# Performance work log

Measured on AMD Instinct MI355X. Metric: run time of the kernel, lower is better.

## Reference

```python
import jax, jax.numpy as jnp
import numpy as np

DIM = 1024
HEADS = 16
HEAD_DIM = DIM // HEADS
DFF = 4 * DIM
BASE_THETA, K_DOP, K_NOR, K_SERO = 0.5, 0.2, 0.15, 0.1
EPS = 1e-5


def _layernorm(x, g, b):
    mu = jnp.mean(x, axis=-1, keepdims=True)
    var = jnp.var(x, axis=-1, keepdims=True)
    return (x - mu) * jax.lax.rsqrt(var + EPS) * g + b


def setup_inputs() -> dict:
    key = jax.random.key(0)
    ks = jax.random.split(key, 16)
    s = 0.02
    d = {
        'x': jax.random.normal(ks[0], (2, 2048, DIM), dtype=jnp.float32),
        'ln1_g': jnp.ones((DIM,), jnp.float32),
        'ln1_b': jnp.zeros((DIM,), jnp.float32),
        'qkv_w': jax.random.normal(ks[1], (DIM, 3 * DIM), jnp.float32) * s,
        'qkv_b': jnp.zeros((3 * DIM,), jnp.float32),
        'proj_w': jax.random.normal(ks[2], (DIM, DIM), jnp.float32) * s,
        'proj_b': jnp.zeros((DIM,), jnp.float32),
        'kq_w': jax.random.normal(ks[3], (DIM, DIM), jnp.float32) * s,
        'kq_b': jnp.zeros((DIM,), jnp.float32),
        'kk_w': jax.random.normal(ks[4], (DIM, DIM), jnp.float32) * s,
        'kk_b': jnp.zeros((DIM,), jnp.float32),
        'kv_w': jax.random.normal(ks[5], (DIM, DIM), jnp.float32) * s,
        'kv_b': jnp.zeros((DIM,), jnp.float32),
        'ko_w': jax.random.normal(ks[6], (DIM, DIM), jnp.float32) * s,
        'ko_b': jnp.zeros((DIM,), jnp.float32),
        'ln2_g': jnp.ones((DIM,), jnp.float32),
        'ln2_b': jnp.zeros((DIM,), jnp.float32),
        'fc1_w': jax.random.normal(ks[7], (DIM, DFF), jnp.float32) * s,
        'fc1_b': jnp.zeros((DFF,), jnp.float32),
        'fc2_w': jax.random.normal(ks[8], (DFF, DIM), jnp.float32) * s,
        'fc2_b': jnp.zeros((DIM,), jnp.float32),
    }
    return d


def _mha(x, qkv_w, qkv_b, proj_w, proj_b):
    B, N, C = x.shape
    qkv = (x @ qkv_w + qkv_b).reshape(B, N, 3, HEADS, HEAD_DIM)
    q, k, v = qkv[:, :, 0], qkv[:, :, 1], qkv[:, :, 2]  # [B,N,H,Hd]
    scale = HEAD_DIM ** -0.5
    attn = jnp.einsum('bnhd,bmhd->bhnm', q, k) * scale
    attn = jax.nn.softmax(attn, axis=-1)
    out = jnp.einsum('bhnm,bmhd->bnhd', attn, v).reshape(B, N, C)
    return out @ proj_w + proj_b


def _kernel_attn(x, kq_w, kq_b, kk_w, kk_b, kv_w, kv_b, ko_w, ko_b):
    q = x @ kq_w + kq_b
    k = x @ kk_w + kk_b
    v = x @ kv_w + kv_b
    qk = jnp.einsum('bnc,bmc->bnm', q, k)
    theta = (BASE_THETA + K_DOP * jax.nn.sigmoid(qk)
             + K_NOR * jnp.tanh(qk) + K_SERO * jax.nn.relu(qk))
    attn = jax.nn.softmax(theta, axis=-1)
    out = jnp.einsum('bnm,bmc->bnc', attn, v)
    return out @ ko_w + ko_b


def reference(x, ln1_g, ln1_b, qkv_w, qkv_b, proj_w, proj_b,
              kq_w, kq_b, kk_w, kk_b, kv_w, kv_b, ko_w, ko_b,
              ln2_g, ln2_b, fc1_w, fc1_b, fc2_w, fc2_b):
    x = x + _mha(_layernorm(x, ln1_g, ln1_b), qkv_w, qkv_b, proj_w, proj_b)
    x = x + _kernel_attn(x, kq_w, kq_b, kk_w, kk_b, kv_w, kv_b, ko_w, ko_b)
    h = _layernorm(x, ln2_g, ln2_b)
    h = jax.nn.gelu(h @ fc1_w + fc1_b, approximate=False) @ fc2_w + fc2_b
    return x + h
```

## Files before the change

### kernel.cpp

```cpp
#include <hip/hip_runtime.h>
#include <math.h>


#define DIMC   1024
#define NTOK   4096
#define SEQ    2048
#define NHEADS 16
#define DFFC   4096
#define QSCALE 0.125f

typedef unsigned short u16;
typedef __attribute__((ext_vector_type(8))) short s16x8;
typedef __attribute__((ext_vector_type(4))) float f32x4;
#define MFMA16(a,b,c) __builtin_amdgcn_mfma_f32_16x16x32_bf16(a,b,c,0,0,0)

__device__ __forceinline__ float b2f(u16 u){ return __uint_as_float(((unsigned int)u)<<16); }
__device__ __forceinline__ u16 f2b(float f){
  unsigned int u = __float_as_uint(f);
  u += 0x7fffu + ((u>>16)&1u);
  return (u16)(u>>16);
}
__device__ __forceinline__ unsigned int pkbf(float a, float b){
  unsigned int r;
  asm("v_cvt_pk_bf16_f32 %0, %1, %2" : "=v"(r) : "v"(a), "v"(b));
  return r;
}
__device__ __forceinline__ float frcp(float x){
  float r;
  asm("v_rcp_f32 %0, %1" : "=v"(r) : "v"(x));
  return r;
}

__device__ __forceinline__ float ldIn(const void* base, long idx, int f32){
  return f32 ? ((const float*)base)[idx] : b2f(((const u16*)base)[idx]);
}
__device__ __forceinline__ float4 ldIn4(const void* base, long idx, int f32){
  if (f32) return *(const float4*)((const float*)base + idx);
  ushort4 u = *(const ushort4*)((const u16*)base + idx);
  return make_float4(b2f(u.x), b2f(u.y), b2f(u.z), b2f(u.w));
}
__device__ __forceinline__ void ld8(const void* base, long idx, int f32, float* v){
  if (f32){
    float4 a = *(const float4*)((const float*)base + idx);
    float4 b = *(const float4*)((const float*)base + idx + 4);
    v[0]=a.x; v[1]=a.y; v[2]=a.z; v[3]=a.w;
    v[4]=b.x; v[5]=b.y; v[6]=b.z; v[7]=b.w;
  } else {
    ushort4 a = *(const ushort4*)((const u16*)base + idx);
    ushort4 b = *(const ushort4*)((const u16*)base + idx + 4);
    v[0]=b2f(a.x); v[1]=b2f(a.y); v[2]=b2f(a.z); v[3]=b2f(a.w);
    v[4]=b2f(b.x); v[5]=b2f(b.y); v[6]=b2f(b.z); v[7]=b2f(b.w);
  }
}
__device__ __forceinline__ void st8(void* base, long idx, int f32, const float* v){
  if (f32){
    *(float4*)((float*)base + idx)     = make_float4(v[0],v[1],v[2],v[3]);
    *(float4*)((float*)base + idx + 4) = make_float4(v[4],v[5],v[6],v[7]);
  } else {
    unsigned int q0 = (unsigned int)f2b(v[0]) | ((unsigned int)f2b(v[1])<<16);
    unsigned int q1 = (unsigned int)f2b(v[2]) | ((unsigned int)f2b(v[3])<<16);
    unsigned int q2 = (unsigned int)f2b(v[4]) | ((unsigned int)f2b(v[5])<<16);
    unsigned int q3 = (unsigned int)f2b(v[6]) | ((unsigned int)f2b(v[7])<<16);
    *(uint4*)((u16*)base + idx) = make_uint4(q0,q1,q2,q3);
  }
}

__device__ __forceinline__ float waveSum(float v){
  #pragma unroll
  for (int off=32; off>0; off>>=1) v += __shfl_xor(v, off, 64);
  return v;
}

__device__ __forceinline__ void async16(const u16* g, u16* l){
  __builtin_amdgcn_global_load_lds(
      (const __attribute__((address_space(1))) unsigned int*)g,
      (__attribute__((address_space(3))) unsigned int*)l, 16, 0, 0);
}

__global__ void detect_kernel(const void* ones, int* flag){
  if (threadIdx.x == 0 && blockIdx.x == 0){
    unsigned int w = *(const unsigned int*)ones;
    *flag = (w == 0x3F803F80u) ? 0 : 1;
  }
}

__global__ __launch_bounds__(256)
void transpose_w(const void* __restrict__ in, u16* __restrict__ out,
                 const int* __restrict__ flagp, int K, int N)
{
  __shared__ u16 t[32][36];
  const int fl = *flagp;
  const int n0 = blockIdx.x*32, k0 = blockIdx.y*32;
  const int tx = threadIdx.x & 31, ty = threadIdx.x >> 5;
  #pragma unroll
  for (int r = ty; r < 32; r += 8)
    t[r][tx] = f2b(ldIn(in, (long)(k0+r)*N + n0 + tx, fl));
  __syncthreads();
  #pragma unroll
  for (int r = ty; r < 32; r += 8)
    out[(long)(n0+r)*K + k0 + tx] = t[tx][r];
}

__global__ __launch_bounds__(256)
void transpose_w3(const void* in0, const void* in1, const void* in2,
                  u16* __restrict__ out, const int* __restrict__ flagp)
{
  __shared__ u16 t[32][36];
  const int fl = *flagp;
  const void* in = (blockIdx.z==0) ? in0 : ((blockIdx.z==1) ? in1 : in2);
  u16* o = out + (long)blockIdx.z*1048576L;
  const int n0 = blockIdx.x*32, k0 = blockIdx.y*32;
  const int tx = threadIdx.x & 31, ty = threadIdx.x >> 5;
  #pragma unroll
  for (int r = ty; r < 32; r += 8)
    t[r][tx] = f2b(ldIn(in, (long)(k0+r)*1024 + n0 + tx, fl));
  __syncthreads();
  #pragma unroll
  for (int r = ty; r < 32; r += 8)
    o[(long)(n0+r)*1024 + k0 + tx] = t[tx][r];
}

template<int BM, int MODE, int ACT, int NW>
__global__ __launch_bounds__(NW*64)
void gemm_mfma(const u16* __restrict__ A, const u16* __restrict__ BT,
               const void* __restrict__ bias, const void* __restrict__ bias2,
               const void* __restrict__ bias3, const void* res,
               void* C, u16* Cv, const int* __restrict__ flagp, int cExt,
               int M, int N, int K, int lda, int ldb, int ldc,
               long sA, long sB, long sC)
{
  constexpr int DEPTH = (BM==128) ? 1 : 3;
  constexpr int BUFS = (BM+128)*64;
  constexpr int ST   = BM*132;
  constexpr int LSZ  = (DEPTH*BUFS > ST) ? DEPTH*BUFS : ST;
  __shared__ u16 lds[LSZ];

  const int fl = *flagp;
  const int fC = cExt ? fl : 0;
  const int z = blockIdx.z;
  A += (long)z*sA; BT += (long)z*sB;
  const long coff = (long)z*sC;
  const int m0 = blockIdx.x*BM, n0 = blockIdx.y*128;
  const int tid = threadIdx.x, w = tid>>6, l = tid&63;
  const int lr = l&15, lq = l>>4;
  constexpr int MW  = (NW==8) ? 4 : 2;
  constexpr int FM  = BM/MW/16;
  constexpr int ANI = BM/8/NW;
  constexpr int BNI = 16/NW;
  constexpr int LCNT= ANI+BNI;
  const int wm = (w&(MW-1))*(BM/MW), wn = (w/MW)*64;

  const int rq = l>>3;
  const int cperm = (l&7) ^ rq;
  const u16* pa = A  + (long)(m0 + rq)*lda + cperm*8;
  const u16* pb = BT + (long)(n0 + rq)*ldb + cperm*8;

  f32x4 acc[FM][4];
  f32x4 osum[FM];
  #pragma unroll
  for (int i=0;i<FM;i++){
    osum[i] = (f32x4){0.f,0.f,0.f,0.f};
    #pragma unroll
    for (int j=0;j<4;j++) acc[i][j] = (f32x4){0.f,0.f,0.f,0.f};
  }

  auto stage = [&](u16* buf){
    u16* As = buf;
    u16* Bs = buf + BM*64;
    #pragma unroll
    for (int p=0;p<ANI;p++){
      const int ia = p*NW + w;
      async16(pa + (long)ia*8*lda, &As[ia*512]);
    }
    #pragma unroll
    for (int p=0;p<BNI;p++){
      const int ib = p*NW + w;
      async16(pb + (long)ib*8*ldb, &Bs[ib*512]);
    }
    pa += 64; pb += 64;
  };

  auto compute = [&](const u16* As){
    const u16* Bs = As + BM*64;
    const int swz = lr & 7;
    #pragma unroll
    for (int h=0; h<2; h++){
      s16x8 af[FM], bf[4];
      const int slot = ((h*4 + lq) ^ swz) << 3;
      #pragma unroll
      for (int i=0;i<FM;i++)
        af[i] = *(const s16x8*)&As[(wm + i*16 + lr)*64 + slot];
      #pragma unroll
      for (int j=0;j<4;j++)
        bf[j] = *(const s16x8*)&Bs[(wn + j*16 + lr)*64 + slot];
      __builtin_amdgcn_s_setprio(1);
      #pragma unroll
      for (int i=0;i<FM;i++)
        #pragma unroll
        for (int j=0;j<4;j++) acc[i][j] = MFMA16(af[i], bf[j], acc[i][j]);
      if constexpr (MODE==5){
        const s16x8 onesv = (s16x8){0x3F80,0x3F80,0x3F80,0x3F80,
                                    0x3F80,0x3F80,0x3F80,0x3F80};
        #pragma unroll
        for (int i=0;i<FM;i++) osum[i] = MFMA16(af[i], onesv, osum[i]);
      }
      __builtin_amdgcn_s_setprio(0);
    }
  };

  const int nk = K >> 6;

  if constexpr (DEPTH == 3){
    auto waitL = [&](){
      if constexpr (LCNT==3)      asm volatile("s_waitcnt vmcnt(3)" ::: "memory");
      else if constexpr (LCNT==6) asm volatile("s_waitcnt vmcnt(6)" ::: "memory");
      else                        asm volatile("s_waitcnt vmcnt(8)" ::: "memory");
      __builtin_amdgcn_s_barrier();
    };
    stage(lds);
    stage(lds + BUFS);
    int cur = 0;
    for (int t = 0; t < nk-2; ++t){
      waitL();
      int nxt = cur+2; if (nxt >= 3) nxt -= 3;
      stage(lds + nxt*BUFS);
      compute(lds + cur*BUFS);
      cur = (cur==2) ? 0 : cur+1;
    }
    waitL();
    compute(lds + cur*BUFS);
    cur = (cur==2) ? 0 : cur+1;
    asm volatile("s_waitcnt vmcnt(0)" ::: "memory");
    __builtin_amdgcn_s_barrier();
    compute(lds + cur*BUFS);
    __syncthreads();
  } else {
    for (int t = 0; t < nk; ++t){
      stage(lds);
      asm volatile("s_waitcnt vmcnt(0)" ::: "memory");
      __builtin_amdgcn_s_barrier();
      compute(lds);
      __syncthreads();
    }
  }

  if constexpr (MODE==5){
    #pragma unroll
    for (int i=0;i<FM;i++)
      #pragma unroll
      for (int r=0;r<4;r++){
        float inv = 1.f / osum[i][r];
        #pragma unroll
        for (int j=0;j<4;j++) acc[i][j][r] *= inv;
      }
  }

  const bool vtr = (MODE==1) && (n0 >= 2048);
  #pragma unroll
  for (int i=0;i<FM;i++)
    #pragma unroll
    for (int j=0;j<4;j++)
      #pragma unroll
      for (int r=0;r<4;r++){
        const u16 bv16 = f2b(acc[i][j][r]);
        if (vtr)
          lds[(wn + j*16 + lr)*132 + wm + i*16 + lq*4 + r] = bv16;
        else
          lds[(wm + i*16 + lq*4 + r)*132 + wn + j*16 + lr] = bv16;
      }
  __syncthreads();

  constexpr int RPP = NW*4;
  const int trow = tid >> 4, tcol = (tid & 15)*8;
  const int gcol = n0 + tcol;

  if (vtr){
    const int bidx = m0 >> 11;
    const int tb = (m0 & 2047) + tcol;
    #pragma unroll
    for (int p=0; p<BM/RPP; p++){
      const int ch = p*RPP + trow;
      float bv = ldIn(bias3, n0 - 2048 + ch, fl);
      float v[8];
      #pragma unroll
      for (int e=0;e<8;e++) v[e] = b2f(lds[ch*132 + tcol + e]) + bv;
      st8(Cv, (long)bidx*2097152L + (long)(n0 - 2048 + ch)*2048 + tb, 0, v);
    }
    return;
  }

  #pragma unroll
  for (int p=0; p<BM/RPP; p++){
    const int row = p*RPP + trow;
    const long grow = m0 + row;
    float v[8];
    #pragma unroll
    for (int e=0;e<8;e++) v[e] = b2f(lds[row*132 + tcol + e]);

    if (MODE == 2){
      #pragma unroll
      for (int e=0;e<8;e++){
        float q = v[e];
        float En = __expf(-q);
        float sig = frcp(1.f + En);
        float t2 = fminf(En*En, 3.0e38f);
        float th = (1.f - t2) * frcp(1.f + t2);
        v[e] = __expf(0.5f + 0.2f*sig + 0.15f*th + 0.1f*fmaxf(q,0.f));
      }
      st8(C, coff + grow*ldc + gcol, 0, v);
    } else if (MODE == 1){
      const void* bb = (n0 < 1024) ? bias : bias2;
      const int cofs = (n0 < 1024) ? 0 : 1024;
      float bv[8]; ld8(bb, gcol - cofs, fl, bv);
      #pragma unroll
      for (int e=0;e<8;e++) v[e] += bv[e];
      st8(C, grow*2048 + gcol, 0, v);
    } else {
      if (bias){
        float bv[8]; ld8(bias, gcol, fl, bv);
        #pragma unroll
        for (int e=0;e<8;e++) v[e] += bv[e];
      }
      if (MODE == 3 && gcol < 1024){
        #pragma unroll
        for (int e=0;e<8;e++) v[e] *= QSCALE;
      }
      if (ACT==1){
        #pragma unroll
        for (int e=0;e<8;e++){
          float u = v[e];
          float y = 1.5957691216f*u*(1.f + 0.044715f*u*u);
          v[e] = u / (1.f + __expf(-y));
        }
      }
      const long idx = coff + grow*ldc + gcol;
      if (res){
        float rv[8]; ld8(res, idx, fl, rv);
        #pragma unroll
        for (int e=0;e<8;e++) v[e] += rv[e];
      }
      st8(C, idx, fC, v);
      if (MODE == 4)
        st8(Cv, grow*1024 + gcol, 0, v);
    }
  }
}

__global__ __launch_bounds__(256)
void ln_kernel(const void* __restrict__ in, const void* __restrict__ g,
               const void* __restrict__ b, u16* __restrict__ outp,
               const int* __restrict__ flagp, int inFlagged)
{
  const int fl = *flagp;
  const int fin = inFlagged ? fl : 0;
  const int row = blockIdx.x;
  const int tid = threadIdx.x;
  float4 xv = ldIn4(in, (long)row*DIMC + tid*4, fin);
  float v0=xv.x, v1=xv.y, v2=xv.z, v3=xv.w;
  float s  = v0+v1+v2+v3;
  float s2 = v0*v0+v1*v1+v2*v2+v3*v3;
  s = waveSum(s); s2 = waveSum(s2);
  __shared__ float sh[8];
  int w = tid>>6, ln = tid&63;
  if (ln==0){ sh[w]=s; sh[4+w]=s2; }
  __syncthreads();
  float ts  = sh[0]+sh[1]+sh[2]+sh[3];
  float ts2 = sh[4]+sh[5]+sh[6]+sh[7];
  float mu  = ts * (1.f/1024.f);
  float var = ts2 * (1.f/1024.f) - mu*mu;
  float rs  = rsqrtf(var + 1e-5f);
  int c = tid*4;
  float4 gv = ldIn4(g, c, fl);
  float4 bv = ldIn4(b, c, fl);
  ushort4 o;
  o.x = f2b((v0-mu)*rs*gv.x + bv.x);
  o.y = f2b((v1-mu)*rs*gv.y + bv.y);
  o.z = f2b((v2-mu)*rs*gv.z + bv.z);
  o.w = f2b((v3-mu)*rs*gv.w + bv.w);
  *(ushort4*)(outp + (long)row*DIMC + c) = o;
}

__global__ __launch_bounds__(512)
void mha_flash(const u16* __restrict__ qkv, u16* __restrict__ outp)
{
  __shared__ u16 Kl[2][64][72];
  __shared__ u16 Vt[2][64][72];
  __shared__ u16 Pl[8][16][72];
  const int h  = blockIdx.y;
  const int bb = blockIdx.z;
  const int q0 = blockIdx.x * 128;
  const int tid = threadIdx.x, lane = tid & 63, w = tid >> 6;
  const int lr = lane & 15, lq = lane >> 4;
  const long tokBase = (long)bb * SEQ;

  s16x8 qf0, qf1;
  {
    const u16* qp = qkv + (tokBase + q0 + w*16 + lr)*3072 + h*64 + lq*8;
    qf0 = *(const s16x8*)qp;
    qf1 = *(const s16x8*)(qp + 32);
  }
  f32x4 o[4];
  #pragma unroll
  for (int d=0;d<4;d++) o[d] = (f32x4){0.f,0.f,0.f,0.f};
  f32x4 osum = (f32x4){0.f,0.f,0.f,0.f};
  const s16x8 onesv = (s16x8){0x3F80,0x3F80,0x3F80,0x3F80,0x3F80,0x3F80,0x3F80,0x3F80};

  const int kk = tid >> 3, kd = (tid & 7) * 8;
  const bool doV = (tid < 256);
  const int p2 = tid & 31, dg = (tid >> 5) & 7;

  uint4 kr, vA, vB;
  const u16* kbase = qkv + (tokBase + kk)*3072 + 1024 + h*64 + kd;
  const u16* vbase = qkv + (tokBase + 2*p2)*3072 + 2048 + h*64 + dg*8;

  auto ldKV = [&](int k0){
    kr = *(const uint4*)(kbase + (long)k0*3072);
    if (doV){
      const u16* vp = vbase + (long)k0*3072;
      vA = *(const uint4*)vp;
      vB = *(const uint4*)(vp + 3072);
    }
  };
  auto wrKV = [&](int bi){
    *(uint4*)&Kl[bi][kk][kd] = kr;
    if (doV){
      unsigned int pk;
      #pragma unroll
      for (int jj=0;jj<4;jj++){
        pk = ((const u16*)&vA)[jj] | ((unsigned int)((const u16*)&vB)[jj] << 16);
        *(unsigned int*)&Vt[bi][dg*8+jj][2*p2] = pk;
        pk = ((const u16*)&vA)[4+jj] | ((unsigned int)((const u16*)&vB)[4+jj] << 16);
        *(unsigned int*)&Vt[bi][dg*8+4+jj][2*p2] = pk;
      }
    }
  };

  ldKV(0);
  int bi = 0;
  for (int k0 = 0; k0 < SEQ; k0 += 64){
    wrKV(bi);
    if (k0 + 64 < SEQ) ldKV(k0 + 64);
    __syncthreads();

    f32x4 s[4];
    #pragma unroll
    for (int c=0;c<4;c++){
      s[c] = (f32x4){0.f,0.f,0.f,0.f};
      s16x8 kf0 = *(const s16x8*)&Kl[bi][c*16+lr][lq*8];
      s16x8 kf1 = *(const s16x8*)&Kl[bi][c*16+lr][lq*8+32];
      __builtin_amdgcn_s_setprio(1);
      s[c] = MFMA16(qf0, kf0, s[c]);
      s[c] = MFMA16(qf1, kf1, s[c]);
      __builtin_amdgcn_s_setprio(0);
    }
    #pragma unroll
    for (int c=0;c<4;c++){
      float p0 = __expf(s[c][0]);
      float p1 = __expf(s[c][1]);
      float p2v = __expf(s[c][2]);
      float p3 = __expf(s[c][3]);
      unsigned int a01 = pkbf(p0, p1);
      unsigned int a23 = pkbf(p2v, p3);
      u16* pr = &Pl[w][lq*4][c*16+lr];
      pr[0]   = (u16)a01;
      pr[72]  = (u16)(a01>>16);
      pr[144] = (u16)a23;
      pr[216] = (u16)(a23>>16);
    }
    s16x8 pf0 = *(const s16x8*)&Pl[w][lr][lq*8];
    s16x8 pf1 = *(const s16x8*)&Pl[w][lr][32+lq*8];
    __builtin_amdgcn_s_setprio(1);
    osum = MFMA16(pf0, onesv, osum);
    osum = MFMA16(pf1, onesv, osum);
    __builtin_amdgcn_s_setprio(0);
    #pragma unroll
    for (int d=0;d<4;d++){
      s16x8 vf0 = *(const s16x8*)&Vt[bi][d*16+lr][lq*8];
      s16x8 vf1 = *(const s16x8*)&Vt[bi][d*16+lr][32+lq*8];
      __builtin_amdgcn_s_setprio(1);
      o[d] = MFMA16(pf0, vf0, o[d]);
      o[d] = MFMA16(pf1, vf1, o[d]);
      __builtin_amdgcn_s_setprio(0);
    }
    bi ^= 1;
  }

  #pragma unroll
  for (int r=0;r<4;r++){
    float inv = 1.f / osum[r];
    long row = (tokBase + q0 + w*16 + lq*4 + r) * (long)DIMC + h*64;
    unsigned int pk01 = pkbf(o[0][r]*inv, o[1][r]*inv);
    unsigned int pk23 = pkbf(o[2][r]*inv, o[3][r]*inv);
    outp[row + lr     ] = (u16)pk01;
    outp[row + lr + 16] = (u16)(pk01>>16);
    outp[row + lr + 32] = (u16)pk23;
    outp[row + lr + 48] = (u16)(pk23>>16);
  }
}

extern "C" void kernel_launch(void* const* d_in, const int* in_sizes, int n_in,
                              void* d_out, int out_size, void* d_ws, size_t ws_size,
                              hipStream_t stream)
{
  const void* x      = d_in[0];
  const void* ln1_g  = d_in[1];
  const void* ln1_b  = d_in[2];
  const void* qkv_w  = d_in[3];
  const void* qkv_b  = d_in[4];
  const void* proj_w = d_in[5];
  const void* proj_b = d_in[6];
  const void* kq_w   = d_in[7];
  const void* kq_b   = d_in[8];
  const void* kk_w   = d_in[9];
  const void* kk_b   = d_in[10];
  const void* kv_w   = d_in[11];
  const void* kv_b   = d_in[12];
  const void* ko_w   = d_in[13];
  const void* ko_b   = d_in[14];
  const void* ln2_g  = d_in[15];
  const void* ln2_b  = d_in[16];
  const void* fc1_w  = d_in[17];
  const void* fc1_b  = d_in[18];
  const void* fc2_w  = d_in[19];
  const void* fc2_b  = d_in[20];

  int* flag = (int*)d_ws;
  u16* Ar   = (u16*)((char*)d_ws + 64);
  u16* B0   = Ar + 4194304L;
  u16* QK   = B0;
  u16* Vt   = B0 + 8388608L;
  u16* C0   = B0 + 12582912L;
  u16* Sb   = C0;
  u16* WT   = C0;
  u16* WT2  = C0 + 4194304L;
  u16* AT   = C0 + 4194304L;
  u16* FC1  = B0;
  u16* Qr   = B0;

  dim3 blk(256);
  const void* np = nullptr;

  detect_kernel<<<1, 64, 0, stream>>>(ln1_g, flag);
  transpose_w<<<dim3(96,32), blk, 0, stream>>>(qkv_w, WT, flag, DIMC, 3*DIMC);
  ln_kernel<<<NTOK, blk, 0, stream>>>(x, ln1_g, ln1_b, Ar, flag, 1);
  gemm_mfma<128,3,0,4><<<dim3(32,24,1), blk, 0, stream>>>(
      Ar, WT, qkv_b, np, np, np, Qr, nullptr, flag, 0,
      NTOK, 3*DIMC, DIMC, DIMC, DIMC, 3*DIMC, 0,0,0);
  mha_flash<<<dim3(SEQ/128, NHEADS, 2), dim3(512), 0, stream>>>(Qr, AT);
  transpose_w<<<dim3(32,32), blk, 0, stream>>>(proj_w, WT, flag, DIMC, DIMC);
  gemm_mfma<64,4,0,8><<<dim3(64,8,1), dim3(512), 0, stream>>>(
      AT, WT, proj_b, np, np, x, d_out, Ar, flag, 1,
      NTOK, DIMC, DIMC, DIMC, DIMC, DIMC, 0,0,0);
  transpose_w3<<<dim3(32,32,3), blk, 0, stream>>>(kq_w, kk_w, kv_w, WT, flag);
  gemm_mfma<128,1,0,4><<<dim3(32,24,1), blk, 0, stream>>>(
      Ar, WT, kq_b, kk_b, kv_b, np, QK, Vt, flag, 0,
      NTOK, 3*DIMC, DIMC, DIMC, DIMC, 2048, 0,0,0);
  gemm_mfma<128,2,0,4><<<dim3(16,16,2), blk, 0, stream>>>(
      QK, QK + 1024, np, np, np, np, Sb, nullptr, flag, 0,
      SEQ, SEQ, DIMC, 2048, 2048, SEQ, 4194304L, 4194304L, 4194304L);
  gemm_mfma<64,5,0,8><<<dim3(32,8,2), dim3(512), 0, stream>>>(
      Sb, Vt, np, np, np, np, Ar, nullptr, flag, 0,
      SEQ, DIMC, SEQ, SEQ, SEQ, DIMC, 4194304L, 2097152L, 2097152L);
  transpose_w<<<dim3(32,32), blk, 0, stream>>>(ko_w, WT, flag, DIMC, DIMC);
  gemm_mfma<64,0,0,8><<<dim3(64,8,1), dim3(512), 0, stream>>>(
      Ar, WT, ko_b, np, np, d_out, d_out, nullptr, flag, 1,
      NTOK, DIMC, DIMC, DIMC, DIMC, DIMC, 0,0,0);
  ln_kernel<<<NTOK, blk, 0, stream>>>(d_out, ln2_g, ln2_b, Ar, flag, 1);
  transpose_w<<<dim3(128,32), blk, 0, stream>>>(fc1_w, WT2, flag, DIMC, DFFC);
  gemm_mfma<128,0,1,4><<<dim3(32,32,1), blk, 0, stream>>>(
      Ar, WT2, fc1_b, np, np, np, FC1, nullptr, flag, 0,
      NTOK, DFFC, DIMC, DIMC, DIMC, DFFC, 0,0,0);
  transpose_w<<<dim3(32,128), blk, 0, stream>>>(fc2_w, WT2, flag, DFFC, DIMC);
  gemm_mfma<64,0,0,8><<<dim3(64,8,1), dim3(512), 0, stream>>>(
      FC1, WT2, fc2_b, np, np, d_out, d_out, nullptr, flag, 1,
      NTOK, DIMC, DFFC, DFFC, DFFC, DIMC, 0,0,0);
}
```

Baseline: 571.6 us.

## Split MHA flash attention over key halves with a separate combine kernel

Splits the attention key range into two halves so the grid doubles from 512 to 1024 blocks. Each half writes unnormalized bf16 partial outputs and row sums to scratch buffers (d_out and Ar are reused), and a new combine kernel adds the halves and normalizes. The goal is better CU occupancy on a grid that was small relative to the GPU. In exchange it adds an extra kernel launch, extra global traffic and bf16 rounding of the partials, and it drops LDS double buffering in favour of two syncs per iteration.

```diff
diff --git a/kernel.cpp b/kernel.cpp
--- a/kernel.cpp
+++ b/kernel.cpp
@@ -381,17 +381,20 @@
 }
 
 __global__ __launch_bounds__(512)
-void mha_flash(const u16* __restrict__ qkv, u16* __restrict__ outp)
+void mha_split(const u16* __restrict__ qkv, u16* __restrict__ p0,
+               u16* __restrict__ p1, float* __restrict__ osums)
 {
-  __shared__ u16 Kl[2][64][72];
-  __shared__ u16 Vt[2][64][72];
+  __shared__ u16 Kl[64][72];
+  __shared__ u16 Vt[64][72];
   __shared__ u16 Pl[8][16][72];
   const int h  = blockIdx.y;
-  const int bb = blockIdx.z;
+  const int bb = blockIdx.z >> 1;
+  const int ks = blockIdx.z & 1;
   const int q0 = blockIdx.x * 128;
   const int tid = threadIdx.x, lane = tid & 63, w = tid >> 6;
   const int lr = lane & 15, lq = lane >> 4;
   const long tokBase = (long)bb * SEQ;
+  const long kBase   = tokBase + ks*1024;
 
   s16x8 qf0, qf1;
   {
@@ -410,8 +413,8 @@
   const int p2 = tid & 31, dg = (tid >> 5) & 7;
 
   uint4 kr, vA, vB;
-  const u16* kbase = qkv + (tokBase + kk)*3072 + 1024 + h*64 + kd;
-  const u16* vbase = qkv + (tokBase + 2*p2)*3072 + 2048 + h*64 + dg*8;
+  const u16* kbase = qkv + (kBase + kk)*3072 + 1024 + h*64 + kd;
+  const u16* vbase = qkv + (kBase + 2*p2)*3072 + 2048 + h*64 + dg*8;
 
   auto ldKV = [&](int k0){
     kr = *(const uint4*)(kbase + (long)k0*3072);
@@ -421,33 +424,33 @@
       vB = *(const uint4*)(vp + 3072);
     }
   };
-  auto wrKV = [&](int bi){
-    *(uint4*)&Kl[bi][kk][kd] = kr;
+  auto wrKV = [&](){
+    *(uint4*)&Kl[kk][kd] = kr;
     if (doV){
       unsigned int pk;
       #pragma unroll
       for (int jj=0;jj<4;jj++){
         pk = ((const u16*)&vA)[jj] | ((unsigned int)((const u16*)&vB)[jj] << 16);
-        *(unsigned int*)&Vt[bi][dg*8+jj][2*p2] = pk;
+        *(unsigned int*)&Vt[dg*8+jj][2*p2] = pk;
         pk = ((const u16*)&vA)[4+jj] | ((unsigned int)((const u16*)&vB)[4+jj] << 16);
-        *(unsigned int*)&Vt[bi][dg*8+4+jj][2*p2] = pk;
+        *(unsigned int*)&Vt[dg*8+4+jj][2*p2] = pk;
       }
     }
   };
 
   ldKV(0);
-  int bi = 0;
-  for (int k0 = 0; k0 < SEQ; k0 += 64){
-    wrKV(bi);
-    if (k0 + 64 < SEQ) ldKV(k0 + 64);
+  for (int k0 = 0; k0 < 1024; k0 += 64){
+    __syncthreads();
+    wrKV();
+    if (k0 + 64 < 1024) ldKV(k0 + 64);
     __syncthreads();
 
     f32x4 s[4];
     #pragma unroll
     for (int c=0;c<4;c++){
       s[c] = (f32x4){0.f,0.f,0.f,0.f};
-      s16x8 kf0 = *(const s16x8*)&Kl[bi][c*16+lr][lq*8];
-      s16x8 kf1 = *(const s16x8*)&Kl[bi][c*16+lr][lq*8+32];
+      s16x8 kf0 = *(const s16x8*)&Kl[c*16+lr][lq*8];
+      s16x8 kf1 = *(const s16x8*)&Kl[c*16+lr][lq*8+32];
       __builtin_amdgcn_s_setprio(1);
       s[c] = MFMA16(qf0, kf0, s[c]);
       s[c] = MFMA16(qf1, kf1, s[c]);
@@ -455,12 +458,12 @@
     }
     #pragma unroll
     for (int c=0;c<4;c++){
-      float p0 = __expf(s[c][0]);
-      float p1 = __expf(s[c][1]);
-      float p2v = __expf(s[c][2]);
-      float p3 = __expf(s[c][3]);
-      unsigned int a01 = pkbf(p0, p1);
-      unsigned int a23 = pkbf(p2v, p3);
+      float e0 = __expf(s[c][0]);
+      float e1 = __expf(s[c][1]);
+      float e2 = __expf(s[c][2]);
+      float e3 = __expf(s[c][3]);
+      unsigned int a01 = pkbf(e0, e1);
+      unsigned int a23 = pkbf(e2, e3);
       u16* pr = &Pl[w][lq*4][c*16+lr];
       pr[0]   = (u16)a01;
       pr[72]  = (u16)(a01>>16);
@@ -475,27 +478,48 @@
     __builtin_amdgcn_s_setprio(0);
     #pragma unroll
     for (int d=0;d<4;d++){
-      s16x8 vf0 = *(const s16x8*)&Vt[bi][d*16+lr][lq*8];
-      s16x8 vf1 = *(const s16x8*)&Vt[bi][d*16+lr][32+lq*8];
+      s16x8 vf0 = *(const s16x8*)&Vt[d*16+lr][lq*8];
+      s16x8 vf1 = *(const s16x8*)&Vt[d*16+lr][32+lq*8];
       __builtin_amdgcn_s_setprio(1);
       o[d] = MFMA16(pf0, vf0, o[d]);
       o[d] = MFMA16(pf1, vf1, o[d]);
       __builtin_amdgcn_s_setprio(0);
     }
-    bi ^= 1;
-  }
-
+  }
+
+  u16* pp = ks ? p1 : p0;
   #pragma unroll
   for (int r=0;r<4;r++){
-    float inv = 1.f / osum[r];
-    long row = (tokBase + q0 + w*16 + lq*4 + r) * (long)DIMC + h*64;
-    unsigned int pk01 = pkbf(o[0][r]*inv, o[1][r]*inv);
-    unsigned int pk23 = pkbf(o[2][r]*inv, o[3][r]*inv);
-    outp[row + lr     ] = (u16)pk01;
-    outp[row + lr + 16] = (u16)(pk01>>16);
-    outp[row + lr + 32] = (u16)pk23;
-    outp[row + lr + 48] = (u16)(pk23>>16);
-  }
+    long row = tokBase + q0 + w*16 + lq*4 + r;
+    long base = row * (long)DIMC + h*64;
+    unsigned int pk01 = pkbf(o[0][r], o[1][r]);
+    unsigned int pk23 = pkbf(o[2][r], o[3][r]);
+    pp[base + lr     ] = (u16)pk01;
+    pp[base + lr + 16] = (u16)(pk01>>16);
+    pp[base + lr + 32] = (u16)pk23;
+    pp[base + lr + 48] = (u16)(pk23>>16);
+    if (lr == 0)
+      osums[((long)ks*4096 + row)*16 + h] = osum[r];
+  }
+}
+
+__global__ __launch_bounds__(256)
+void mha_combine(const u16* __restrict__ p0, const u16* __restrict__ p1,
+                 const float* __restrict__ osums, u16* __restrict__ outp)
+{
+  const long row = blockIdx.x;
+  const int c = threadIdx.x * 4;
+  const int h = c >> 6;
+  float s = osums[row*16 + h] + osums[(4096 + row)*16 + h];
+  float inv = 1.f / s;
+  ushort4 a = *(const ushort4*)(p0 + row*DIMC + c);
+  ushort4 b = *(const ushort4*)(p1 + row*DIMC + c);
+  ushort4 o;
+  o.x = f2b((b2f(a.x)+b2f(b.x))*inv);
+  o.y = f2b((b2f(a.y)+b2f(b.y))*inv);
+  o.z = f2b((b2f(a.z)+b2f(b.z))*inv);
+  o.w = f2b((b2f(a.w)+b2f(b.w))*inv);
+  *(ushort4*)(outp + row*DIMC + c) = o;
 }
 
 extern "C" void kernel_launch(void* const* d_in, const int* in_sizes, int n_in,
@@ -536,6 +560,7 @@
   u16* AT   = C0 + 4194304L;
   u16* FC1  = B0;
   u16* Qr   = B0;
+  float* OS = (float*)C0;
 
   dim3 blk(256);
   const void* np = nullptr;
@@ -546,7 +571,9 @@
   gemm_mfma<128,3,0,4><<<dim3(32,24,1), blk, 0, stream>>>(
       Ar, WT, qkv_b, np, np, np, Qr, nullptr, flag, 0,
       NTOK, 3*DIMC, DIMC, DIMC, DIMC, 3*DIMC, 0,0,0);
-  mha_flash<<<dim3(SEQ/128, NHEADS, 2), dim3(512), 0, stream>>>(Qr, AT);
+  mha_split<<<dim3(SEQ/128, NHEADS, 4), dim3(512), 0, stream>>>(
+      Qr, (u16*)d_out, Ar, OS);
+  mha_combine<<<dim3(NTOK), blk, 0, stream>>>((u16*)d_out, Ar, OS, AT);
   transpose_w<<<dim3(32,32), blk, 0, stream>>>(proj_w, WT, flag, DIMC, DIMC);
   gemm_mfma<64,4,0,8><<<dim3(64,8,1), dim3(512), 0, stream>>>(
       AT, WT, proj_b, np, np, x, d_out, Ar, flag, 1,
```

Result: slower. 643.6 us (+12.6%).
